# Performance work log

Hardware: AMD Instinct MI355X
Metric: run time of the kernel (lower is better)

Reference implementation:

```python
import jax, jax.numpy as jnp
import numpy as np

FFT_SIZE = 2046
MSE_WEIGHT = 0.7
DELAY_WEIGHT = 0.3
ENERGY_EPS = 1e-8
RANGE_EPS = 1e-8
TEMP_SCALE = 10.0


def setup_inputs() -> dict:
    key = jax.random.key(0)
    k1, k2 = jax.random.split(key)
    shape = (32, 64, 4, 1024)  # [batch, bs_ant, ue_ant, subcarriers]
    predicted_csi = jax.random.normal(k1, shape, dtype=jnp.float32)
    target_csi = jax.random.normal(k2, shape, dtype=jnp.float32)
    return {"predicted_csi": predicted_csi, "target_csi": target_csi}


def _compute_pdp(csi):
    # Real input is treated as complex with zero imaginary part (as in torch module).
    n = csi.shape[-1]
    if n < FFT_SIZE:
        pad = [(0, 0)] * (csi.ndim - 1) + [(0, FFT_SIZE - n)]
        csi = jnp.pad(csi, pad)
    else:
        csi = csi[..., :FFT_SIZE]
    td = jnp.fft.ifft(csi.astype(jnp.complex64), axis=-1)  # [..., FFT_SIZE]
    return jnp.abs(td) ** 2


def _normalize_pdp(pdp):
    # Per-sample (last-axis) energy normalization; skip if energy ~ 0.
    energy = jnp.sum(pdp, axis=-1, keepdims=True)
    return jnp.where(energy < ENERGY_EPS, pdp, pdp / energy)


def _soft_delay(pdp):
    # Adaptive-temperature soft-argmax delay per sample.
    f = pdp.shape[-1]
    idx = jnp.arange(f, dtype=jnp.float32)
    rng = jnp.clip(jnp.max(pdp, -1, keepdims=True) - jnp.min(pdp, -1, keepdims=True), RANGE_EPS)
    weights = jax.nn.softmax(pdp * (TEMP_SCALE / rng), axis=-1)
    return jnp.sum(idx * weights, axis=-1)


def reference(predicted_csi, target_csi):
    pdp_pred = _normalize_pdp(_compute_pdp(predicted_csi))  # [B, BS, UE, FFT_SIZE]
    pdp_tgt = _normalize_pdp(_compute_pdp(target_csi))
    # MSE per sample is mean over FFT_SIZE; averaging over samples/antenna pairs == global mean.
    mse_loss = jnp.mean((pdp_pred - pdp_tgt) ** 2)
    delay_diff = jnp.abs(_soft_delay(pdp_pred) - _soft_delay(pdp_tgt)) / FFT_SIZE
    delay_loss = jnp.mean(delay_diff)
    return MSE_WEIGHT * mse_loss + DELAY_WEIGHT * delay_loss
```

## Files before the change

### kernel.cpp

```cpp
#include <hip/hip_runtime.h>
#include <math.h>

#define IN_N   1024
#define NROWS  8192
#define NTOT   16384
#define FFT_N  2046

typedef unsigned short u16;
typedef __attribute__((ext_vector_type(8))) __bf16 bf16x8;
typedef __attribute__((ext_vector_type(4))) float  f32x4;

__device__ __forceinline__ u16 f2bf(float f) {
    unsigned u = __builtin_bit_cast(unsigned, f);
    unsigned r = (u + 0x7fffu + ((u >> 16) & 1u)) >> 16;
    return (u16)r;
}
__device__ __forceinline__ float bf2f(u16 h) {
    unsigned u = ((unsigned)h) << 16;
    return __builtin_bit_cast(float, u);
}

__device__ __forceinline__ void gload_lds16(const void* g, void* l) {
    __builtin_amdgcn_global_load_lds(
        (__attribute__((address_space(1))) void*)g,
        (__attribute__((address_space(3))) void*)l, 16, 0, 0);
}

__global__ void twiddle_kernel(u16* __restrict__ Wc, u16* __restrict__ Ws) {
    int k = blockIdx.x;
    int n0 = threadIdx.x * 4;
    const float c = 6.28318530717958647692f / 2046.0f;
    ushort4 oc, os;
    #pragma unroll
    for (int i = 0; i < 4; ++i) {
        int n = n0 + i;
        int m = (k * n) % FFT_N;
        float a = (float)m * c;
        float sv, cv;
        __sincosf(a, &sv, &cv);
        ((u16*)&oc)[i] = f2bf(cv);
        ((u16*)&os)[i] = f2bf(sv);
    }
    size_t o = (size_t)k * IN_N + n0;
    *(ushort4*)(Wc + o) = oc;
    *(ushort4*)(Ws + o) = os;
}

__global__ __launch_bounds__(256) void convert_kernel(
    const float* __restrict__ pred, const float* __restrict__ tgt,
    u16* __restrict__ Xh) {
    size_t gid = (size_t)blockIdx.x * 256 + threadIdx.x;
    size_t e = gid * 4;
    const size_t half = (size_t)NROWS * IN_N;
    const float* s = (e < half) ? (pred + e) : (tgt + (e - half));
    float4 v = *(const float4*)s;
    ushort4 o;
    o.x = f2bf(v.x); o.y = f2bf(v.y); o.z = f2bf(v.z); o.w = f2bf(v.w);
    *(ushort4*)(Xh + e) = o;
}

#define BM 128
#define BN 256
#define BK 32
#define NKT 32

#define FENCE() asm volatile("" ::: "memory")

__global__ __launch_bounds__(512, 2) void dft_pdp_mfma(
    const u16* __restrict__ Wc, const u16* __restrict__ Ws,
    const u16* __restrict__ Xh, u16* __restrict__ pdp) {

    __shared__ __align__(16) char lds[2][32768];

    const int bid  = blockIdx.x;
    const int xcd  = bid & 7;
    const int slot = bid >> 3;
    const int m0 = (slot & 7) * BM;
    const int r0 = (xcd * 8 + (slot >> 3)) * BN;

    const int t    = threadIdx.x;
    const int w    = t >> 6;
    const int lane = t & 63;
    const int wm = (w & 1) * 64;
    const int wr = (w >> 1) * 64;
    const int lr = lane & 15;
    const int rdoff = (((lane >> 4) ^ ((lane >> 1) & 3)) << 4);

    const int srow  = t >> 2;
    const int sslot = (t & 3) ^ ((t >> 3) & 3);
    const size_t aOfs  = (size_t)(m0 + srow) * 2048 + sslot * 16;
    const size_t xOfs0 = (size_t)(r0 + srow) * 2048 + sslot * 16;
    const size_t xOfs1 = (size_t)(r0 + 128 + srow) * 2048 + sslot * 16;
    const int woff = w << 10;

    f32x4 accRe[4][4], accIm[4][4];
    #pragma unroll
    for (int i = 0; i < 4; ++i)
        #pragma unroll
        for (int j = 0; j < 4; ++j)
            #pragma unroll
            for (int q = 0; q < 4; ++q) { accRe[i][j][q] = 0.f; accIm[i][j][q] = 0.f; }

    #define STAGE_A(buf, kt) do { \
        gload_lds16((const char*)Wc + aOfs + (size_t)(kt) * 64, &lds[buf][0] + woff); \
        gload_lds16((const char*)Ws + aOfs + (size_t)(kt) * 64, &lds[buf][0] + 8192 + woff); \
    } while (0)
    #define STAGE_X(buf, kt) do { \
        gload_lds16((const char*)Xh + xOfs0 + (size_t)(kt) * 64, &lds[buf][0] + 16384 + woff); \
        gload_lds16((const char*)Xh + xOfs1 + (size_t)(kt) * 64, &lds[buf][0] + 24576 + woff); \
    } while (0)
    #define LDA(buf, off) (*(const bf16x8*)(&lds[buf][0] + (wm + (off) + lr) * 64 + rdoff))
    #define LDSN(buf, off) (*(const bf16x8*)(&lds[buf][0] + 8192 + (wm + (off) + lr) * 64 + rdoff))
    #define LDX(buf, j)   (*(const bf16x8*)(&lds[buf][0] + 16384 + (wr + (j) * 16 + lr) * 64 + rdoff))

    STAGE_A(0, 0); STAGE_X(0, 0);
    asm volatile("s_waitcnt vmcnt(0)" ::: "memory");
    __builtin_amdgcn_s_barrier();
    FENCE();

    bf16x8 fb0, fb1, fb2, fb3, fa0, fa1, fa2, fa3, fs0, fs1, fs2, fs3;
    fb0 = LDX(0, 0); fb1 = LDX(0, 1); fb2 = LDX(0, 2); fb3 = LDX(0, 3);
    fa0 = LDA(0, 0); fa1 = LDA(0, 16); fs0 = LDSN(0, 0); fs1 = LDSN(0, 16);

    for (int kt = 0; kt < NKT; ++kt) {
        const int cur  = kt & 1;
        const int nb   = cur ^ 1;
        const bool more = (kt + 1) < NKT;

        fa2 = LDA(cur, 32); fa3 = LDA(cur, 48);
        fs2 = LDSN(cur, 32); fs3 = LDSN(cur, 48);
        if (more) STAGE_A(nb, kt + 1);
        asm volatile("s_waitcnt lgkmcnt(4)" ::: "memory");
        __builtin_amdgcn_sched_barrier(0);
        __builtin_amdgcn_s_setprio(1);
        accRe[0][0] = __builtin_amdgcn_mfma_f32_16x16x32_bf16(fa0, fb0, accRe[0][0], 0, 0, 0);
        accIm[0][0] = __builtin_amdgcn_mfma_f32_16x16x32_bf16(fs0, fb0, accIm[0][0], 0, 0, 0);
        accRe[0][1] = __builtin_amdgcn_mfma_f32_16x16x32_bf16(fa0, fb1, accRe[0][1], 0, 0, 0);
        accIm[0][1] = __builtin_amdgcn_mfma_f32_16x16x32_bf16(fs0, fb1, accIm[0][1], 0, 0, 0);
        accRe[0][2] = __builtin_amdgcn_mfma_f32_16x16x32_bf16(fa0, fb2, accRe[0][2], 0, 0, 0);
        accIm[0][2] = __builtin_amdgcn_mfma_f32_16x16x32_bf16(fs0, fb2, accIm[0][2], 0, 0, 0);
        accRe[0][3] = __builtin_amdgcn_mfma_f32_16x16x32_bf16(fa0, fb3, accRe[0][3], 0, 0, 0);
        accIm[0][3] = __builtin_amdgcn_mfma_f32_16x16x32_bf16(fs0, fb3, accIm[0][3], 0, 0, 0);
        accRe[1][0] = __builtin_amdgcn_mfma_f32_16x16x32_bf16(fa1, fb0, accRe[1][0], 0, 0, 0);
        accIm[1][0] = __builtin_amdgcn_mfma_f32_16x16x32_bf16(fs1, fb0, accIm[1][0], 0, 0, 0);
        accRe[1][1] = __builtin_amdgcn_mfma_f32_16x16x32_bf16(fa1, fb1, accRe[1][1], 0, 0, 0);
        accIm[1][1] = __builtin_amdgcn_mfma_f32_16x16x32_bf16(fs1, fb1, accIm[1][1], 0, 0, 0);
        accRe[1][2] = __builtin_amdgcn_mfma_f32_16x16x32_bf16(fa1, fb2, accRe[1][2], 0, 0, 0);
        accIm[1][2] = __builtin_amdgcn_mfma_f32_16x16x32_bf16(fs1, fb2, accIm[1][2], 0, 0, 0);
        accRe[1][3] = __builtin_amdgcn_mfma_f32_16x16x32_bf16(fa1, fb3, accRe[1][3], 0, 0, 0);
        accIm[1][3] = __builtin_amdgcn_mfma_f32_16x16x32_bf16(fs1, fb3, accIm[1][3], 0, 0, 0);
        __builtin_amdgcn_s_setprio(0);

        if (more) STAGE_X(nb, kt + 1);
        asm volatile("s_waitcnt lgkmcnt(0)" ::: "memory");
        __builtin_amdgcn_sched_barrier(0);
        __builtin_amdgcn_s_setprio(1);
        accRe[2][0] = __builtin_amdgcn_mfma_f32_16x16x32_bf16(fa2, fb0, accRe[2][0], 0, 0, 0);
        accIm[2][0] = __builtin_amdgcn_mfma_f32_16x16x32_bf16(fs2, fb0, accIm[2][0], 0, 0, 0);
        accRe[2][1] = __builtin_amdgcn_mfma_f32_16x16x32_bf16(fa2, fb1, accRe[2][1], 0, 0, 0);
        accIm[2][1] = __builtin_amdgcn_mfma_f32_16x16x32_bf16(fs2, fb1, accIm[2][1], 0, 0, 0);
        accRe[2][2] = __builtin_amdgcn_mfma_f32_16x16x32_bf16(fa2, fb2, accRe[2][2], 0, 0, 0);
        accIm[2][2] = __builtin_amdgcn_mfma_f32_16x16x32_bf16(fs2, fb2, accIm[2][2], 0, 0, 0);
        accRe[2][3] = __builtin_amdgcn_mfma_f32_16x16x32_bf16(fa2, fb3, accRe[2][3], 0, 0, 0);
        accIm[2][3] = __builtin_amdgcn_mfma_f32_16x16x32_bf16(fs2, fb3, accIm[2][3], 0, 0, 0);
        accRe[3][0] = __builtin_amdgcn_mfma_f32_16x16x32_bf16(fa3, fb0, accRe[3][0], 0, 0, 0);
        accIm[3][0] = __builtin_amdgcn_mfma_f32_16x16x32_bf16(fs3, fb0, accIm[3][0], 0, 0, 0);
        accRe[3][1] = __builtin_amdgcn_mfma_f32_16x16x32_bf16(fa3, fb1, accRe[3][1], 0, 0, 0);
        accIm[3][1] = __builtin_amdgcn_mfma_f32_16x16x32_bf16(fs3, fb1, accIm[3][1], 0, 0, 0);
        accRe[3][2] = __builtin_amdgcn_mfma_f32_16x16x32_bf16(fa3, fb2, accRe[3][2], 0, 0, 0);
        accIm[3][2] = __builtin_amdgcn_mfma_f32_16x16x32_bf16(fs3, fb2, accIm[3][2], 0, 0, 0);
        accRe[3][3] = __builtin_amdgcn_mfma_f32_16x16x32_bf16(fa3, fb3, accRe[3][3], 0, 0, 0);
        accIm[3][3] = __builtin_amdgcn_mfma_f32_16x16x32_bf16(fs3, fb3, accIm[3][3], 0, 0, 0);
        __builtin_amdgcn_s_setprio(0);

        if (more) {
            asm volatile("s_waitcnt vmcnt(0)" ::: "memory");
            __builtin_amdgcn_s_barrier();
            FENCE();
            fb0 = LDX(nb, 0); fb1 = LDX(nb, 1); fb2 = LDX(nb, 2); fb3 = LDX(nb, 3);
            fa0 = LDA(nb, 0); fa1 = LDA(nb, 16);
            fs0 = LDSN(nb, 0); fs1 = LDSN(nb, 16);
        }
    }
    #undef STAGE_A
    #undef STAGE_X
    #undef LDA
    #undef LDSN
    #undef LDX

    const float inv = 1.0f / ((float)FFT_N * (float)FFT_N);
    #pragma unroll
    for (int i = 0; i < 4; ++i)
        #pragma unroll
        for (int j = 0; j < 4; ++j) {
            int m = m0 + wm + i * 16 + (lane >> 4) * 4;
            int r = r0 + wr + j * 16 + (lane & 15);
            ushort4 o;
            #pragma unroll
            for (int q = 0; q < 4; ++q) {
                float re = accRe[i][j][q], im = accIm[i][j][q];
                ((u16*)&o)[q] = f2bf((re * re + im * im) * inv);
            }
            *(ushort4*)(pdp + (size_t)r * IN_N + m) = o;
        }
}

__device__ __forceinline__ float wsum(float v) {
    #pragma unroll
    for (int m = 32; m >= 1; m >>= 1) v += __shfl_xor(v, m);
    return v;
}
__device__ __forceinline__ float wmax(float v) {
    #pragma unroll
    for (int m = 32; m >= 1; m >>= 1) v = fmaxf(v, __shfl_xor(v, m));
    return v;
}
__device__ __forceinline__ float wmin(float v) {
    #pragma unroll
    for (int m = 32; m >= 1; m >>= 1) v = fminf(v, __shfl_xor(v, m));
    return v;
}

__global__ __launch_bounds__(256) void row_stats_kernel(
    const u16* __restrict__ pdp,
    float* __restrict__ mse_rows, float* __restrict__ dd_rows) {

    const int wid  = threadIdx.x >> 6;
    const int lane = threadIdx.x & 63;
    const int r = blockIdx.x * 4 + wid;
    const u16* pp = pdp + (size_t)r * IN_N + lane * 16;
    const u16* pt = pdp + (size_t)(NROWS + r) * IN_N + lane * 16;

    uint4 v0 = *(const uint4*)pp;       uint4 v1 = *(const uint4*)(pp + 8);
    uint4 u0 = *(const uint4*)pt;       uint4 u1 = *(const uint4*)(pt + 8);
    float a[16], b[16];
    {
        unsigned pw[8] = {v0.x, v0.y, v0.z, v0.w, v1.x, v1.y, v1.z, v1.w};
        unsigned tw[8] = {u0.x, u0.y, u0.z, u0.w, u1.x, u1.y, u1.z, u1.w};
        #pragma unroll
        for (int i = 0; i < 8; ++i) {
            a[2*i]   = bf2f((u16)(pw[i] & 0xffffu));
            a[2*i+1] = bf2f((u16)(pw[i] >> 16));
            b[2*i]   = bf2f((u16)(tw[i] & 0xffffu));
            b[2*i+1] = bf2f((u16)(tw[i] >> 16));
        }
    }

    float wsp = 0.f, wst = 0.f;
    float mxp = -1e30f, mnp = 1e30f, mxt = -1e30f, mnt = 1e30f;
    #pragma unroll
    for (int i = 0; i < 16; ++i) {
        int k = lane * 16 + i;
        float wgt = (k == 0 || k == 1023) ? 1.f : 2.f;
        wsp += wgt * a[i];        wst += wgt * b[i];
        mxp = fmaxf(mxp, a[i]);   mnp = fminf(mnp, a[i]);
        mxt = fmaxf(mxt, b[i]);   mnt = fminf(mnt, b[i]);
    }
    float Ep  = wsum(wsp);
    float Et  = wsum(wst);
    float Mp  = wmax(mxp);
    float mp_ = wmin(mnp);
    float Mt  = wmax(mxt);
    float mt_ = wmin(mnt);

    float scp = (Ep < 1e-8f) ? 1.f : 1.f / Ep;
    float sct = (Et < 1e-8f) ? 1.f : 1.f / Et;
    float rngp = fmaxf(scp * (Mp - mp_), 1e-8f);
    float rngt = fmaxf(sct * (Mt - mt_), 1e-8f);
    float cfp = 10.f * scp / rngp;
    float cft = 10.f * sct / rngt;
    float smp = cfp * Mp;
    float smt = cft * Mt;

    float zp = 0.f, zt = 0.f, ms = 0.f;
    #pragma unroll
    for (int i = 0; i < 16; ++i) {
        int k = lane * 16 + i;
        float wgt = (k == 0 || k == 1023) ? 1.f : 2.f;
        zp += wgt * __expf(cfp * a[i] - smp);
        zt += wgt * __expf(cft * b[i] - smt);
        float d = a[i] * scp - b[i] * sct;
        ms += wgt * d * d;
    }
    float Zp  = wsum(zp);
    float Zt  = wsum(zt);
    float MSE = wsum(ms);

    if (lane == 0) {
        float w0p = __expf(cfp * a[0] - smp) / Zp;
        float w0t = __expf(cft * b[0] - smt) / Zt;
        mse_rows[r] = MSE;
        dd_rows[r]  = 0.5f * fabsf(w0p - w0t);
    }
}

__global__ __launch_bounds__(256) void final_kernel(
    const float* __restrict__ mse_rows, const float* __restrict__ dd_rows,
    float* __restrict__ out) {
    __shared__ float r1[256];
    __shared__ float r2[256];
    int t = threadIdx.x;
    float s1 = 0.f, s2 = 0.f;
    for (int r = t; r < NROWS; r += 256) { s1 += mse_rows[r]; s2 += dd_rows[r]; }
    r1[t] = s1; r2[t] = s2;
    __syncthreads();
    for (int s = 128; s > 0; s >>= 1) {
        if (t < s) { r1[t] += r1[t + s]; r2[t] += r2[t + s]; }
        __syncthreads();
    }
    if (t == 0) {
        float mse = r1[0] / ((float)NROWS * (float)FFT_N);
        float dl  = r2[0] / (float)NROWS;
        out[0] = 0.7f * mse + 0.3f * dl;
    }
}

extern "C" void kernel_launch(void* const* d_in, const int* in_sizes, int n_in,
                              void* d_out, int out_size, void* d_ws, size_t ws_size,
                              hipStream_t stream) {
    const float* pred = (const float*)d_in[0];
    const float* tgt  = (const float*)d_in[1];
    float* out = (float*)d_out;

    char* ws = (char*)d_ws;
    u16* Xh   = (u16*)ws;
    u16* Wch  = (u16*)(ws + (size_t)32 * 1024 * 1024);
    u16* Wsh  = (u16*)(ws + (size_t)34 * 1024 * 1024);
    u16* pdp  = (u16*)(ws + (size_t)40 * 1024 * 1024);
    float* mse_rows = (float*)(ws + (size_t)72 * 1024 * 1024);
    float* dd_rows  = mse_rows + NROWS;

    twiddle_kernel<<<1024, 256, 0, stream>>>(Wch, Wsh);
    convert_kernel<<<NTOT * IN_N / 4 / 256, 256, 0, stream>>>(pred, tgt, Xh);

    dft_pdp_mfma<<<512, 512, 0, stream>>>(Wch, Wsh, Xh, pdp);

    row_stats_kernel<<<NROWS / 4, 256, 0, stream>>>(pdp, mse_rows, dd_rows);
    final_kernel<<<1, 256, 0, stream>>>(mse_rows, dd_rows, out);
}
```

Measured before the change: 113.7 us.

## Load X fragments directly to registers and shrink DFT block to 128x128

The DFT GEMM block tile drops from 128x256 with 512 threads to 128x128 with 256 threads, and the grid doubles to 1024 blocks. The X operand is no longer staged through LDS. Each wave loads its B fragments straight from global memory into registers, double-buffered across an unrolled pair of k-steps, while only the twiddle matrices go through LDS. This cuts LDS traffic and footprint and should allow higher occupancy, but it adds uncoalesced 16-byte global loads of X and gives each block less reuse of the twiddle tiles.

```diff
diff --git a/kernel.cpp b/kernel.cpp
--- a/kernel.cpp
+++ b/kernel.cpp
@@ -60,23 +60,23 @@
 }
 
 #define BM 128
-#define BN 256
+#define BN 128
 #define BK 32
 #define NKT 32
 
 #define FENCE() asm volatile("" ::: "memory")
 
-__global__ __launch_bounds__(512, 2) void dft_pdp_mfma(
+__global__ __launch_bounds__(256, 2) void dft_pdp_mfma(
     const u16* __restrict__ Wc, const u16* __restrict__ Ws,
     const u16* __restrict__ Xh, u16* __restrict__ pdp) {
 
-    __shared__ __align__(16) char lds[2][32768];
+    __shared__ __align__(16) char lds[2][16384];
 
     const int bid  = blockIdx.x;
     const int xcd  = bid & 7;
     const int slot = bid >> 3;
     const int m0 = (slot & 7) * BM;
-    const int r0 = (xcd * 8 + (slot >> 3)) * BN;
+    const int r0 = (xcd * 16 + (slot >> 3)) * BN;
 
     const int t    = threadIdx.x;
     const int w    = t >> 6;
@@ -88,10 +88,14 @@
 
     const int srow  = t >> 2;
     const int sslot = (t & 3) ^ ((t >> 3) & 3);
-    const size_t aOfs  = (size_t)(m0 + srow) * 2048 + sslot * 16;
-    const size_t xOfs0 = (size_t)(r0 + srow) * 2048 + sslot * 16;
-    const size_t xOfs1 = (size_t)(r0 + 128 + srow) * 2048 + sslot * 16;
+    const size_t aOfs0 = (size_t)(m0 + srow) * 2048 + sslot * 16;
+    const size_t aOfs1 = aOfs0 + (size_t)64 * 2048;
     const int woff = w << 10;
+
+    const u16* pX0 = Xh + (size_t)(r0 + wr +  0 + lr) * IN_N + (lane >> 4) * 8;
+    const u16* pX1 = Xh + (size_t)(r0 + wr + 16 + lr) * IN_N + (lane >> 4) * 8;
+    const u16* pX2 = Xh + (size_t)(r0 + wr + 32 + lr) * IN_N + (lane >> 4) * 8;
+    const u16* pX3 = Xh + (size_t)(r0 + wr + 48 + lr) * IN_N + (lane >> 4) * 8;
 
     f32x4 accRe[4][4], accIm[4][4];
     #pragma unroll
@@ -101,92 +105,98 @@
             #pragma unroll
             for (int q = 0; q < 4; ++q) { accRe[i][j][q] = 0.f; accIm[i][j][q] = 0.f; }
 
-    #define STAGE_A(buf, kt) do { \
-        gload_lds16((const char*)Wc + aOfs + (size_t)(kt) * 64, &lds[buf][0] + woff); \
-        gload_lds16((const char*)Ws + aOfs + (size_t)(kt) * 64, &lds[buf][0] + 8192 + woff); \
+    #define STAGE(buf, kt) do { \
+        gload_lds16((const char*)Wc + aOfs0 + (size_t)(kt) * 64, &lds[buf][0] + woff); \
+        gload_lds16((const char*)Wc + aOfs1 + (size_t)(kt) * 64, &lds[buf][0] + 4096 + woff); \
+        gload_lds16((const char*)Ws + aOfs0 + (size_t)(kt) * 64, &lds[buf][0] + 8192 + woff); \
+        gload_lds16((const char*)Ws + aOfs1 + (size_t)(kt) * 64, &lds[buf][0] + 12288 + woff); \
     } while (0)
-    #define STAGE_X(buf, kt) do { \
-        gload_lds16((const char*)Xh + xOfs0 + (size_t)(kt) * 64, &lds[buf][0] + 16384 + woff); \
-        gload_lds16((const char*)Xh + xOfs1 + (size_t)(kt) * 64, &lds[buf][0] + 24576 + woff); \
-    } while (0)
-    #define LDA(buf, off) (*(const bf16x8*)(&lds[buf][0] + (wm + (off) + lr) * 64 + rdoff))
+    #define LDA(buf, off)  (*(const bf16x8*)(&lds[buf][0] + (wm + (off) + lr) * 64 + rdoff))
     #define LDSN(buf, off) (*(const bf16x8*)(&lds[buf][0] + 8192 + (wm + (off) + lr) * 64 + rdoff))
-    #define LDX(buf, j)   (*(const bf16x8*)(&lds[buf][0] + 16384 + (wr + (j) * 16 + lr) * 64 + rdoff))
-
-    STAGE_A(0, 0); STAGE_X(0, 0);
+
+    bf16x8 fbE0, fbE1, fbE2, fbE3;
+    bf16x8 fbO0, fbO1, fbO2, fbO3;
+    bf16x8 fa0, fa1, fa2, fa3, fs0, fs1, fs2, fs3;
+
+    STAGE(0, 0);
+    fbE0 = *(const bf16x8*)(pX0); fbE1 = *(const bf16x8*)(pX1);
+    fbE2 = *(const bf16x8*)(pX2); fbE3 = *(const bf16x8*)(pX3);
     asm volatile("s_waitcnt vmcnt(0)" ::: "memory");
     __builtin_amdgcn_s_barrier();
     FENCE();
-
-    bf16x8 fb0, fb1, fb2, fb3, fa0, fa1, fa2, fa3, fs0, fs1, fs2, fs3;
-    fb0 = LDX(0, 0); fb1 = LDX(0, 1); fb2 = LDX(0, 2); fb3 = LDX(0, 3);
     fa0 = LDA(0, 0); fa1 = LDA(0, 16); fs0 = LDSN(0, 0); fs1 = LDSN(0, 16);
 
-    for (int kt = 0; kt < NKT; ++kt) {
-        const int cur  = kt & 1;
-        const int nb   = cur ^ 1;
-        const bool more = (kt + 1) < NKT;
-
-        fa2 = LDA(cur, 32); fa3 = LDA(cur, 48);
-        fs2 = LDSN(cur, 32); fs3 = LDSN(cur, 48);
-        if (more) STAGE_A(nb, kt + 1);
-        asm volatile("s_waitcnt lgkmcnt(4)" ::: "memory");
-        __builtin_amdgcn_sched_barrier(0);
-        __builtin_amdgcn_s_setprio(1);
-        accRe[0][0] = __builtin_amdgcn_mfma_f32_16x16x32_bf16(fa0, fb0, accRe[0][0], 0, 0, 0);
-        accIm[0][0] = __builtin_amdgcn_mfma_f32_16x16x32_bf16(fs0, fb0, accIm[0][0], 0, 0, 0);
-        accRe[0][1] = __builtin_amdgcn_mfma_f32_16x16x32_bf16(fa0, fb1, accRe[0][1], 0, 0, 0);
-        accIm[0][1] = __builtin_amdgcn_mfma_f32_16x16x32_bf16(fs0, fb1, accIm[0][1], 0, 0, 0);
-        accRe[0][2] = __builtin_amdgcn_mfma_f32_16x16x32_bf16(fa0, fb2, accRe[0][2], 0, 0, 0);
-        accIm[0][2] = __builtin_amdgcn_mfma_f32_16x16x32_bf16(fs0, fb2, accIm[0][2], 0, 0, 0);
-        accRe[0][3] = __builtin_amdgcn_mfma_f32_16x16x32_bf16(fa0, fb3, accRe[0][3], 0, 0, 0);
-        accIm[0][3] = __builtin_amdgcn_mfma_f32_16x16x32_bf16(fs0, fb3, accIm[0][3], 0, 0, 0);
-        accRe[1][0] = __builtin_amdgcn_mfma_f32_16x16x32_bf16(fa1, fb0, accRe[1][0], 0, 0, 0);
-        accIm[1][0] = __builtin_amdgcn_mfma_f32_16x16x32_bf16(fs1, fb0, accIm[1][0], 0, 0, 0);
-        accRe[1][1] = __builtin_amdgcn_mfma_f32_16x16x32_bf16(fa1, fb1, accRe[1][1], 0, 0, 0);
-        accIm[1][1] = __builtin_amdgcn_mfma_f32_16x16x32_bf16(fs1, fb1, accIm[1][1], 0, 0, 0);
-        accRe[1][2] = __builtin_amdgcn_mfma_f32_16x16x32_bf16(fa1, fb2, accRe[1][2], 0, 0, 0);
-        accIm[1][2] = __builtin_amdgcn_mfma_f32_16x16x32_bf16(fs1, fb2, accIm[1][2], 0, 0, 0);
-        accRe[1][3] = __builtin_amdgcn_mfma_f32_16x16x32_bf16(fa1, fb3, accRe[1][3], 0, 0, 0);
-        accIm[1][3] = __builtin_amdgcn_mfma_f32_16x16x32_bf16(fs1, fb3, accIm[1][3], 0, 0, 0);
-        __builtin_amdgcn_s_setprio(0);
-
-        if (more) STAGE_X(nb, kt + 1);
-        asm volatile("s_waitcnt lgkmcnt(0)" ::: "memory");
-        __builtin_amdgcn_sched_barrier(0);
-        __builtin_amdgcn_s_setprio(1);
-        accRe[2][0] = __builtin_amdgcn_mfma_f32_16x16x32_bf16(fa2, fb0, accRe[2][0], 0, 0, 0);
-        accIm[2][0] = __builtin_amdgcn_mfma_f32_16x16x32_bf16(fs2, fb0, accIm[2][0], 0, 0, 0);
-        accRe[2][1] = __builtin_amdgcn_mfma_f32_16x16x32_bf16(fa2, fb1, accRe[2][1], 0, 0, 0);
-        accIm[2][1] = __builtin_amdgcn_mfma_f32_16x16x32_bf16(fs2, fb1, accIm[2][1], 0, 0, 0);
-        accRe[2][2] = __builtin_amdgcn_mfma_f32_16x16x32_bf16(fa2, fb2, accRe[2][2], 0, 0, 0);
-        accIm[2][2] = __builtin_amdgcn_mfma_f32_16x16x32_bf16(fs2, fb2, accIm[2][2], 0, 0, 0);
-        accRe[2][3] = __builtin_amdgcn_mfma_f32_16x16x32_bf16(fa2, fb3, accRe[2][3], 0, 0, 0);
-        accIm[2][3] = __builtin_amdgcn_mfma_f32_16x16x32_bf16(fs2, fb3, accIm[2][3], 0, 0, 0);
-        accRe[3][0] = __builtin_amdgcn_mfma_f32_16x16x32_bf16(fa3, fb0, accRe[3][0], 0, 0, 0);
-        accIm[3][0] = __builtin_amdgcn_mfma_f32_16x16x32_bf16(fs3, fb0, accIm[3][0], 0, 0, 0);
-        accRe[3][1] = __builtin_amdgcn_mfma_f32_16x16x32_bf16(fa3, fb1, accRe[3][1], 0, 0, 0);
-        accIm[3][1] = __builtin_amdgcn_mfma_f32_16x16x32_bf16(fs3, fb1, accIm[3][1], 0, 0, 0);
-        accRe[3][2] = __builtin_amdgcn_mfma_f32_16x16x32_bf16(fa3, fb2, accRe[3][2], 0, 0, 0);
-        accIm[3][2] = __builtin_amdgcn_mfma_f32_16x16x32_bf16(fs3, fb2, accIm[3][2], 0, 0, 0);
-        accRe[3][3] = __builtin_amdgcn_mfma_f32_16x16x32_bf16(fa3, fb3, accRe[3][3], 0, 0, 0);
-        accIm[3][3] = __builtin_amdgcn_mfma_f32_16x16x32_bf16(fs3, fb3, accIm[3][3], 0, 0, 0);
-        __builtin_amdgcn_s_setprio(0);
-
-        if (more) {
-            asm volatile("s_waitcnt vmcnt(0)" ::: "memory");
-            __builtin_amdgcn_s_barrier();
-            FENCE();
-            fb0 = LDX(nb, 0); fb1 = LDX(nb, 1); fb2 = LDX(nb, 2); fb3 = LDX(nb, 3);
-            fa0 = LDA(nb, 0); fa1 = LDA(nb, 16);
-            fs0 = LDSN(nb, 0); fs1 = LDSN(nb, 16);
-        }
-    }
-    #undef STAGE_A
-    #undef STAGE_X
+    #define TILE(kt, CUR, NB, FBC0, FBC1, FBC2, FBC3, FBN0, FBN1, FBN2, FBN3) do { \
+        const bool more_ = (kt + 1) < NKT; \
+         \
+        fa2 = LDA(CUR, 32); fa3 = LDA(CUR, 48); \
+        fs2 = LDSN(CUR, 32); fs3 = LDSN(CUR, 48); \
+        if (more_) { \
+            FBN0 = *(const bf16x8*)(pX0 + (kt + 1) * 32); \
+            FBN1 = *(const bf16x8*)(pX1 + (kt + 1) * 32); \
+            FBN2 = *(const bf16x8*)(pX2 + (kt + 1) * 32); \
+            FBN3 = *(const bf16x8*)(pX3 + (kt + 1) * 32); \
+            STAGE(NB, kt + 1); \
+        } \
+        asm volatile("s_waitcnt lgkmcnt(4)" ::: "memory");    \
+        __builtin_amdgcn_sched_barrier(0); \
+        __builtin_amdgcn_s_setprio(1); \
+        accRe[0][0] = __builtin_amdgcn_mfma_f32_16x16x32_bf16(fa0, FBC0, accRe[0][0], 0, 0, 0); \
+        accIm[0][0] = __builtin_amdgcn_mfma_f32_16x16x32_bf16(fs0, FBC0, accIm[0][0], 0, 0, 0); \
+        accRe[0][1] = __builtin_amdgcn_mfma_f32_16x16x32_bf16(fa0, FBC1, accRe[0][1], 0, 0, 0); \
+        accIm[0][1] = __builtin_amdgcn_mfma_f32_16x16x32_bf16(fs0, FBC1, accIm[0][1], 0, 0, 0); \
+        accRe[0][2] = __builtin_amdgcn_mfma_f32_16x16x32_bf16(fa0, FBC2, accRe[0][2], 0, 0, 0); \
+        accIm[0][2] = __builtin_amdgcn_mfma_f32_16x16x32_bf16(fs0, FBC2, accIm[0][2], 0, 0, 0); \
+        accRe[0][3] = __builtin_amdgcn_mfma_f32_16x16x32_bf16(fa0, FBC3, accRe[0][3], 0, 0, 0); \
+        accIm[0][3] = __builtin_amdgcn_mfma_f32_16x16x32_bf16(fs0, FBC3, accIm[0][3], 0, 0, 0); \
+        accRe[1][0] = __builtin_amdgcn_mfma_f32_16x16x32_bf16(fa1, FBC0, accRe[1][0], 0, 0, 0); \
+        accIm[1][0] = __builtin_amdgcn_mfma_f32_16x16x32_bf16(fs1, FBC0, accIm[1][0], 0, 0, 0); \
+        accRe[1][1] = __builtin_amdgcn_mfma_f32_16x16x32_bf16(fa1, FBC1, accRe[1][1], 0, 0, 0); \
+        accIm[1][1] = __builtin_amdgcn_mfma_f32_16x16x32_bf16(fs1, FBC1, accIm[1][1], 0, 0, 0); \
+        accRe[1][2] = __builtin_amdgcn_mfma_f32_16x16x32_bf16(fa1, FBC2, accRe[1][2], 0, 0, 0); \
+        accIm[1][2] = __builtin_amdgcn_mfma_f32_16x16x32_bf16(fs1, FBC2, accIm[1][2], 0, 0, 0); \
+        accRe[1][3] = __builtin_amdgcn_mfma_f32_16x16x32_bf16(fa1, FBC3, accRe[1][3], 0, 0, 0); \
+        accIm[1][3] = __builtin_amdgcn_mfma_f32_16x16x32_bf16(fs1, FBC3, accIm[1][3], 0, 0, 0); \
+        __builtin_amdgcn_s_setprio(0); \
+         \
+        asm volatile("s_waitcnt lgkmcnt(0)" ::: "memory");    \
+        __builtin_amdgcn_sched_barrier(0); \
+        __builtin_amdgcn_s_setprio(1); \
+        accRe[2][0] = __builtin_amdgcn_mfma_f32_16x16x32_bf16(fa2, FBC0, accRe[2][0], 0, 0, 0); \
+        accIm[2][0] = __builtin_amdgcn_mfma_f32_16x16x32_bf16(fs2, FBC0, accIm[2][0], 0, 0, 0); \
+        accRe[2][1] = __builtin_amdgcn_mfma_f32_16x16x32_bf16(fa2, FBC1, accRe[2][1], 0, 0, 0); \
+        accIm[2][1] = __builtin_amdgcn_mfma_f32_16x16x32_bf16(fs2, FBC1, accIm[2][1], 0, 0, 0); \
+        accRe[2][2] = __builtin_amdgcn_mfma_f32_16x16x32_bf16(fa2, FBC2, accRe[2][2], 0, 0, 0); \
+        accIm[2][2] = __builtin_amdgcn_mfma_f32_16x16x32_bf16(fs2, FBC2, accIm[2][2], 0, 0, 0); \
+        accRe[2][3] = __builtin_amdgcn_mfma_f32_16x16x32_bf16(fa2, FBC3, accRe[2][3], 0, 0, 0); \
+        accIm[2][3] = __builtin_amdgcn_mfma_f32_16x16x32_bf16(fs2, FBC3, accIm[2][3], 0, 0, 0); \
+        accRe[3][0] = __builtin_amdgcn_mfma_f32_16x16x32_bf16(fa3, FBC0, accRe[3][0], 0, 0, 0); \
+        accIm[3][0] = __builtin_amdgcn_mfma_f32_16x16x32_bf16(fs3, FBC0, accIm[3][0], 0, 0, 0); \
+        accRe[3][1] = __builtin_amdgcn_mfma_f32_16x16x32_bf16(fa3, FBC1, accRe[3][1], 0, 0, 0); \
+        accIm[3][1] = __builtin_amdgcn_mfma_f32_16x16x32_bf16(fs3, FBC1, accIm[3][1], 0, 0, 0); \
+        accRe[3][2] = __builtin_amdgcn_mfma_f32_16x16x32_bf16(fa3, FBC2, accRe[3][2], 0, 0, 0); \
+        accIm[3][2] = __builtin_amdgcn_mfma_f32_16x16x32_bf16(fs3, FBC2, accIm[3][2], 0, 0, 0); \
+        accRe[3][3] = __builtin_amdgcn_mfma_f32_16x16x32_bf16(fa3, FBC3, accRe[3][3], 0, 0, 0); \
+        accIm[3][3] = __builtin_amdgcn_mfma_f32_16x16x32_bf16(fs3, FBC3, accIm[3][3], 0, 0, 0); \
+        __builtin_amdgcn_s_setprio(0); \
+         \
+        if (more_) { \
+            asm volatile("s_waitcnt vmcnt(0)" ::: "memory"); \
+            __builtin_amdgcn_s_barrier(); \
+            FENCE(); \
+            fa0 = LDA(NB, 0); fa1 = LDA(NB, 16); \
+            fs0 = LDSN(NB, 0); fs1 = LDSN(NB, 16); \
+        } \
+    } while (0)
+
+    for (int kt2 = 0; kt2 < NKT; kt2 += 2) {
+        TILE(kt2,     0, 1, fbE0, fbE1, fbE2, fbE3, fbO0, fbO1, fbO2, fbO3);
+        TILE(kt2 + 1, 1, 0, fbO0, fbO1, fbO2, fbO3, fbE0, fbE1, fbE2, fbE3);
+    }
+    #undef TILE
+    #undef STAGE
     #undef LDA
     #undef LDSN
-    #undef LDX
 
     const float inv = 1.0f / ((float)FFT_N * (float)FFT_N);
     #pragma unroll
@@ -333,7 +343,7 @@
     twiddle_kernel<<<1024, 256, 0, stream>>>(Wch, Wsh);
     convert_kernel<<<NTOT * IN_N / 4 / 256, 256, 0, stream>>>(pred, tgt, Xh);
 
-    dft_pdp_mfma<<<512, 512, 0, stream>>>(Wch, Wsh, Xh, pdp);
+    dft_pdp_mfma<<<1024, 256, 0, stream>>>(Wch, Wsh, Xh, pdp);
 
     row_stats_kernel<<<NROWS / 4, 256, 0, stream>>>(pdp, mse_rows, dd_rows);
     final_kernel<<<1, 256, 0, stream>>>(mse_rows, dd_rows, out);
```

Result: slower. 136.5 us (+20.1%).

## Shrink DFT GEMM tile to 128x128 with 256 threads and fuse prep kernels

Applied to the files above, without the earlier changes.

Merges the twiddle-generation and bf16 conversion kernels into one launch, removing a kernel boundary. Halves the DFT GEMM block tile along the row dimension (BN 256→128), with 4 waves per block instead of 8 and twice as many blocks. Staging is reworked so each thread loads two A/S rows and two X rows per k-step, and LDS shrinks to 48KB. This trades more global traffic on the twiddle matrix for more blocks and smaller LDS per block, which may improve occupancy or load balance.

```diff
diff --git a/kernel.cpp b/kernel.cpp
--- a/kernel.cpp
+++ b/kernel.cpp
@@ -26,57 +26,58 @@
         (__attribute__((address_space(3))) void*)l, 16, 0, 0);
 }
 
-__global__ void twiddle_kernel(u16* __restrict__ Wc, u16* __restrict__ Ws) {
-    int k = blockIdx.x;
-    int n0 = threadIdx.x * 4;
-    const float c = 6.28318530717958647692f / 2046.0f;
-    ushort4 oc, os;
-    #pragma unroll
-    for (int i = 0; i < 4; ++i) {
-        int n = n0 + i;
-        int m = (k * n) % FFT_N;
-        float a = (float)m * c;
-        float sv, cv;
-        __sincosf(a, &sv, &cv);
-        ((u16*)&oc)[i] = f2bf(cv);
-        ((u16*)&os)[i] = f2bf(sv);
-    }
-    size_t o = (size_t)k * IN_N + n0;
-    *(ushort4*)(Wc + o) = oc;
-    *(ushort4*)(Ws + o) = os;
-}
-
-__global__ __launch_bounds__(256) void convert_kernel(
+__global__ __launch_bounds__(256) void prep_kernel(
     const float* __restrict__ pred, const float* __restrict__ tgt,
-    u16* __restrict__ Xh) {
-    size_t gid = (size_t)blockIdx.x * 256 + threadIdx.x;
-    size_t e = gid * 4;
-    const size_t half = (size_t)NROWS * IN_N;
-    const float* s = (e < half) ? (pred + e) : (tgt + (e - half));
-    float4 v = *(const float4*)s;
-    ushort4 o;
-    o.x = f2bf(v.x); o.y = f2bf(v.y); o.z = f2bf(v.z); o.w = f2bf(v.w);
-    *(ushort4*)(Xh + e) = o;
+    u16* __restrict__ Wc, u16* __restrict__ Ws, u16* __restrict__ Xh) {
+    int bid = blockIdx.x;
+    if (bid < 1024) {
+        int k = bid;
+        int n0 = threadIdx.x * 4;
+        const float c = 6.28318530717958647692f / 2046.0f;
+        ushort4 oc, os;
+        #pragma unroll
+        for (int i = 0; i < 4; ++i) {
+            int n = n0 + i;
+            int m = (k * n) % FFT_N;
+            float a = (float)m * c;
+            float sv, cv;
+            __sincosf(a, &sv, &cv);
+            ((u16*)&oc)[i] = f2bf(cv);
+            ((u16*)&os)[i] = f2bf(sv);
+        }
+        size_t o = (size_t)k * IN_N + n0;
+        *(ushort4*)(Wc + o) = oc;
+        *(ushort4*)(Ws + o) = os;
+    } else {
+        size_t gid = (size_t)(bid - 1024) * 256 + threadIdx.x;
+        size_t e = gid * 4;
+        const size_t half = (size_t)NROWS * IN_N;
+        const float* s = (e < half) ? (pred + e) : (tgt + (e - half));
+        float4 v = *(const float4*)s;
+        ushort4 o;
+        o.x = f2bf(v.x); o.y = f2bf(v.y); o.z = f2bf(v.z); o.w = f2bf(v.w);
+        *(ushort4*)(Xh + e) = o;
+    }
 }
 
 #define BM 128
-#define BN 256
+#define BN 128
 #define BK 32
 #define NKT 32
 
 #define FENCE() asm volatile("" ::: "memory")
 
-__global__ __launch_bounds__(512, 2) void dft_pdp_mfma(
+__global__ __launch_bounds__(256, 2) void dft_pdp_mfma(
     const u16* __restrict__ Wc, const u16* __restrict__ Ws,
     const u16* __restrict__ Xh, u16* __restrict__ pdp) {
 
-    __shared__ __align__(16) char lds[2][32768];
+    __shared__ __align__(16) char lds[2][24576];
 
     const int bid  = blockIdx.x;
     const int xcd  = bid & 7;
     const int slot = bid >> 3;
     const int m0 = (slot & 7) * BM;
-    const int r0 = (xcd * 8 + (slot >> 3)) * BN;
+    const int r0 = (xcd * 16 + (slot >> 3)) * BN;
 
     const int t    = threadIdx.x;
     const int w    = t >> 6;
@@ -88,9 +89,10 @@
 
     const int srow  = t >> 2;
     const int sslot = (t & 3) ^ ((t >> 3) & 3);
-    const size_t aOfs  = (size_t)(m0 + srow) * 2048 + sslot * 16;
+    const size_t aOfs0 = (size_t)(m0 + srow) * 2048 + sslot * 16;
+    const size_t aOfs1 = aOfs0 + (size_t)64 * 2048;
     const size_t xOfs0 = (size_t)(r0 + srow) * 2048 + sslot * 16;
-    const size_t xOfs1 = (size_t)(r0 + 128 + srow) * 2048 + sslot * 16;
+    const size_t xOfs1 = xOfs0 + (size_t)64 * 2048;
     const int woff = w << 10;
 
     f32x4 accRe[4][4], accIm[4][4];
@@ -101,76 +103,61 @@
             #pragma unroll
             for (int q = 0; q < 4; ++q) { accRe[i][j][q] = 0.f; accIm[i][j][q] = 0.f; }
 
-    #define STAGE_A(buf, kt) do { \
-        gload_lds16((const char*)Wc + aOfs + (size_t)(kt) * 64, &lds[buf][0] + woff); \
-        gload_lds16((const char*)Ws + aOfs + (size_t)(kt) * 64, &lds[buf][0] + 8192 + woff); \
+    #define STAGE_AS(buf, kt) do { \
+        gload_lds16((const char*)Wc + aOfs0 + (size_t)(kt) * 64, &lds[buf][0] + woff); \
+        gload_lds16((const char*)Wc + aOfs1 + (size_t)(kt) * 64, &lds[buf][0] + 4096 + woff); \
+        gload_lds16((const char*)Ws + aOfs0 + (size_t)(kt) * 64, &lds[buf][0] + 8192 + woff); \
+        gload_lds16((const char*)Ws + aOfs1 + (size_t)(kt) * 64, &lds[buf][0] + 12288 + woff); \
     } while (0)
     #define STAGE_X(buf, kt) do { \
         gload_lds16((const char*)Xh + xOfs0 + (size_t)(kt) * 64, &lds[buf][0] + 16384 + woff); \
-        gload_lds16((const char*)Xh + xOfs1 + (size_t)(kt) * 64, &lds[buf][0] + 24576 + woff); \
+        gload_lds16((const char*)Xh + xOfs1 + (size_t)(kt) * 64, &lds[buf][0] + 20480 + woff); \
     } while (0)
-    #define LDA(buf, off) (*(const bf16x8*)(&lds[buf][0] + (wm + (off) + lr) * 64 + rdoff))
+    #define LDA(buf, off)  (*(const bf16x8*)(&lds[buf][0] + (wm + (off) + lr) * 64 + rdoff))
     #define LDSN(buf, off) (*(const bf16x8*)(&lds[buf][0] + 8192 + (wm + (off) + lr) * 64 + rdoff))
-    #define LDX(buf, j)   (*(const bf16x8*)(&lds[buf][0] + 16384 + (wr + (j) * 16 + lr) * 64 + rdoff))
-
-    STAGE_A(0, 0); STAGE_X(0, 0);
+    #define LDX(buf, j)    (*(const bf16x8*)(&lds[buf][0] + 16384 + (wr + (j) * 16 + lr) * 64 + rdoff))
+
+    bf16x8 fb0, fb1, fb2, fb3, fa0, fa1, fa2, fa3, fs0, fs1, fs2, fs3;
+
+    #define CLUSTER(i, FA, FS) do { \
+        accRe[i][0] = __builtin_amdgcn_mfma_f32_16x16x32_bf16(FA, fb0, accRe[i][0], 0, 0, 0); \
+        accIm[i][0] = __builtin_amdgcn_mfma_f32_16x16x32_bf16(FS, fb0, accIm[i][0], 0, 0, 0); \
+        accRe[i][1] = __builtin_amdgcn_mfma_f32_16x16x32_bf16(FA, fb1, accRe[i][1], 0, 0, 0); \
+        accIm[i][1] = __builtin_amdgcn_mfma_f32_16x16x32_bf16(FS, fb1, accIm[i][1], 0, 0, 0); \
+        accRe[i][2] = __builtin_amdgcn_mfma_f32_16x16x32_bf16(FA, fb2, accRe[i][2], 0, 0, 0); \
+        accIm[i][2] = __builtin_amdgcn_mfma_f32_16x16x32_bf16(FS, fb2, accIm[i][2], 0, 0, 0); \
+        accRe[i][3] = __builtin_amdgcn_mfma_f32_16x16x32_bf16(FA, fb3, accRe[i][3], 0, 0, 0); \
+        accIm[i][3] = __builtin_amdgcn_mfma_f32_16x16x32_bf16(FS, fb3, accIm[i][3], 0, 0, 0); \
+    } while (0)
+
+    STAGE_AS(0, 0); STAGE_X(0, 0);
     asm volatile("s_waitcnt vmcnt(0)" ::: "memory");
     __builtin_amdgcn_s_barrier();
     FENCE();
-
-    bf16x8 fb0, fb1, fb2, fb3, fa0, fa1, fa2, fa3, fs0, fs1, fs2, fs3;
     fb0 = LDX(0, 0); fb1 = LDX(0, 1); fb2 = LDX(0, 2); fb3 = LDX(0, 3);
     fa0 = LDA(0, 0); fa1 = LDA(0, 16); fs0 = LDSN(0, 0); fs1 = LDSN(0, 16);
 
     for (int kt = 0; kt < NKT; ++kt) {
-        const int cur  = kt & 1;
-        const int nb   = cur ^ 1;
+        const int cur = kt & 1;
+        const int nb  = cur ^ 1;
         const bool more = (kt + 1) < NKT;
 
         fa2 = LDA(cur, 32); fa3 = LDA(cur, 48);
         fs2 = LDSN(cur, 32); fs3 = LDSN(cur, 48);
-        if (more) STAGE_A(nb, kt + 1);
+        if (more) STAGE_AS(nb, kt + 1);
         asm volatile("s_waitcnt lgkmcnt(4)" ::: "memory");
         __builtin_amdgcn_sched_barrier(0);
         __builtin_amdgcn_s_setprio(1);
-        accRe[0][0] = __builtin_amdgcn_mfma_f32_16x16x32_bf16(fa0, fb0, accRe[0][0], 0, 0, 0);
-        accIm[0][0] = __builtin_amdgcn_mfma_f32_16x16x32_bf16(fs0, fb0, accIm[0][0], 0, 0, 0);
-        accRe[0][1] = __builtin_amdgcn_mfma_f32_16x16x32_bf16(fa0, fb1, accRe[0][1], 0, 0, 0);
-        accIm[0][1] = __builtin_amdgcn_mfma_f32_16x16x32_bf16(fs0, fb1, accIm[0][1], 0, 0, 0);
-        accRe[0][2] = __builtin_amdgcn_mfma_f32_16x16x32_bf16(fa0, fb2, accRe[0][2], 0, 0, 0);
-        accIm[0][2] = __builtin_amdgcn_mfma_f32_16x16x32_bf16(fs0, fb2, accIm[0][2], 0, 0, 0);
-        accRe[0][3] = __builtin_amdgcn_mfma_f32_16x16x32_bf16(fa0, fb3, accRe[0][3], 0, 0, 0);
-        accIm[0][3] = __builtin_amdgcn_mfma_f32_16x16x32_bf16(fs0, fb3, accIm[0][3], 0, 0, 0);
-        accRe[1][0] = __builtin_amdgcn_mfma_f32_16x16x32_bf16(fa1, fb0, accRe[1][0], 0, 0, 0);
-        accIm[1][0] = __builtin_amdgcn_mfma_f32_16x16x32_bf16(fs1, fb0, accIm[1][0], 0, 0, 0);
-        accRe[1][1] = __builtin_amdgcn_mfma_f32_16x16x32_bf16(fa1, fb1, accRe[1][1], 0, 0, 0);
-        accIm[1][1] = __builtin_amdgcn_mfma_f32_16x16x32_bf16(fs1, fb1, accIm[1][1], 0, 0, 0);
-        accRe[1][2] = __builtin_amdgcn_mfma_f32_16x16x32_bf16(fa1, fb2, accRe[1][2], 0, 0, 0);
-        accIm[1][2] = __builtin_amdgcn_mfma_f32_16x16x32_bf16(fs1, fb2, accIm[1][2], 0, 0, 0);
-        accRe[1][3] = __builtin_amdgcn_mfma_f32_16x16x32_bf16(fa1, fb3, accRe[1][3], 0, 0, 0);
-        accIm[1][3] = __builtin_amdgcn_mfma_f32_16x16x32_bf16(fs1, fb3, accIm[1][3], 0, 0, 0);
+        CLUSTER(0, fa0, fs0);
+        CLUSTER(1, fa1, fs1);
         __builtin_amdgcn_s_setprio(0);
 
         if (more) STAGE_X(nb, kt + 1);
         asm volatile("s_waitcnt lgkmcnt(0)" ::: "memory");
         __builtin_amdgcn_sched_barrier(0);
         __builtin_amdgcn_s_setprio(1);
-        accRe[2][0] = __builtin_amdgcn_mfma_f32_16x16x32_bf16(fa2, fb0, accRe[2][0], 0, 0, 0);
-        accIm[2][0] = __builtin_amdgcn_mfma_f32_16x16x32_bf16(fs2, fb0, accIm[2][0], 0, 0, 0);
-        accRe[2][1] = __builtin_amdgcn_mfma_f32_16x16x32_bf16(fa2, fb1, accRe[2][1], 0, 0, 0);
-        accIm[2][1] = __builtin_amdgcn_mfma_f32_16x16x32_bf16(fs2, fb1, accIm[2][1], 0, 0, 0);
-        accRe[2][2] = __builtin_amdgcn_mfma_f32_16x16x32_bf16(fa2, fb2, accRe[2][2], 0, 0, 0);
-        accIm[2][2] = __builtin_amdgcn_mfma_f32_16x16x32_bf16(fs2, fb2, accIm[2][2], 0, 0, 0);
-        accRe[2][3] = __builtin_amdgcn_mfma_f32_16x16x32_bf16(fa2, fb3, accRe[2][3], 0, 0, 0);
-        accIm[2][3] = __builtin_amdgcn_mfma_f32_16x16x32_bf16(fs2, fb3, accIm[2][3], 0, 0, 0);
-        accRe[3][0] = __builtin_amdgcn_mfma_f32_16x16x32_bf16(fa3, fb0, accRe[3][0], 0, 0, 0);
-        accIm[3][0] = __builtin_amdgcn_mfma_f32_16x16x32_bf16(fs3, fb0, accIm[3][0], 0, 0, 0);
-        accRe[3][1] = __builtin_amdgcn_mfma_f32_16x16x32_bf16(fa3, fb1, accRe[3][1], 0, 0, 0);
-        accIm[3][1] = __builtin_amdgcn_mfma_f32_16x16x32_bf16(fs3, fb1, accIm[3][1], 0, 0, 0);
-        accRe[3][2] = __builtin_amdgcn_mfma_f32_16x16x32_bf16(fa3, fb2, accRe[3][2], 0, 0, 0);
-        accIm[3][2] = __builtin_amdgcn_mfma_f32_16x16x32_bf16(fs3, fb2, accIm[3][2], 0, 0, 0);
-        accRe[3][3] = __builtin_amdgcn_mfma_f32_16x16x32_bf16(fa3, fb3, accRe[3][3], 0, 0, 0);
-        accIm[3][3] = __builtin_amdgcn_mfma_f32_16x16x32_bf16(fs3, fb3, accIm[3][3], 0, 0, 0);
+        CLUSTER(2, fa2, fs2);
+        CLUSTER(3, fa3, fs3);
         __builtin_amdgcn_s_setprio(0);
 
         if (more) {
@@ -182,8 +169,9 @@
             fs0 = LDSN(nb, 0); fs1 = LDSN(nb, 16);
         }
     }
-    #undef STAGE_A
+    #undef STAGE_AS
     #undef STAGE_X
+    #undef CLUSTER
     #undef LDA
     #undef LDSN
     #undef LDX
@@ -330,10 +318,9 @@
     float* mse_rows = (float*)(ws + (size_t)72 * 1024 * 1024);
     float* dd_rows  = mse_rows + NROWS;
 
-    twiddle_kernel<<<1024, 256, 0, stream>>>(Wch, Wsh);
-    convert_kernel<<<NTOT * IN_N / 4 / 256, 256, 0, stream>>>(pred, tgt, Xh);
-
-    dft_pdp_mfma<<<512, 512, 0, stream>>>(Wch, Wsh, Xh, pdp);
+    prep_kernel<<<1024 + NTOT * IN_N / 4 / 256, 256, 0, stream>>>(pred, tgt, Wch, Wsh, Xh);
+
+    dft_pdp_mfma<<<1024, 256, 0, stream>>>(Wch, Wsh, Xh, pdp);
 
     row_stats_kernel<<<NROWS / 4, 256, 0, stream>>>(pdp, mse_rows, dd_rows);
     final_kernel<<<1, 256, 0, stream>>>(mse_rows, dd_rows, out);
```

Result: faster. 111.3 us (-2.1%).
